# Performance work log

Hardware: AMD Instinct MI355X
Metric: run time of the kernel (lower is better)

The kernel has to match this reference:

```python
import jax, jax.numpy as jnp
import numpy as np

N_HEADS = 16
N_KV_HEADS = 4
N_EMBED = 2048
HEAD_DIM = 128
SECTIONS = [16, 24, 24, 16, 24, 24]


def _process_rotary(c):
    # c: [3, B, T, HEAD_DIM] -> [B, 1, T, HEAD_DIM]
    splits = np.cumsum(SECTIONS)[:-1]
    secs = jnp.split(c, splits, axis=-1)
    out = jnp.concatenate([s[i % 3] for i, s in enumerate(secs)], axis=-1)
    return out[:, None]  # add head axis


def _rotate_half(x):
    x1, x2 = jnp.split(x, 2, axis=-1)
    return jnp.concatenate([-x2, x1], axis=-1)


def setup_inputs() -> dict:
    key = jax.random.key(0)
    ks = jax.random.split(key, 12)
    B, T = 1, 2048
    s = 0.02
    return {
        "x": jax.random.normal(ks[0], (B, T, N_EMBED), jnp.float32),
        "cos": jax.random.uniform(ks[1], (3, B, T, HEAD_DIM), jnp.float32),
        "sin": jax.random.uniform(ks[2], (3, B, T, HEAD_DIM), jnp.float32),
        "Wq": jax.random.normal(ks[3], (N_EMBED, N_EMBED), jnp.float32) * s,
        "bq": jax.random.normal(ks[4], (N_EMBED,), jnp.float32) * s,
        "Wk": jax.random.normal(ks[5], (N_EMBED, N_KV_HEADS * HEAD_DIM), jnp.float32) * s,
        "bk": jax.random.normal(ks[6], (N_KV_HEADS * HEAD_DIM,), jnp.float32) * s,
        "Wv": jax.random.normal(ks[7], (N_EMBED, N_KV_HEADS * HEAD_DIM), jnp.float32) * s,
        "bv": jax.random.normal(ks[8], (N_KV_HEADS * HEAD_DIM,), jnp.float32) * s,
        "Wo": jax.random.normal(ks[9], (N_EMBED, N_EMBED), jnp.float32) * s,
    }


def reference(x, cos, sin, Wq, bq, Wk, bk, Wv, bv, Wo):
    B, T, C = x.shape
    H, Hkv, D = N_HEADS, N_KV_HEADS, HEAD_DIM
    q = (x @ Wq + bq).reshape(B, T, H, D).transpose(0, 2, 1, 3)    # [B,H,T,D]
    k = (x @ Wk + bk).reshape(B, T, Hkv, D).transpose(0, 2, 1, 3)  # [B,Hkv,T,D]
    v = (x @ Wv + bv).reshape(B, T, Hkv, D).transpose(0, 2, 1, 3)
    # multi-section rope (cos/sin are 4-dim -> custom path)
    c = _process_rotary(cos)
    s = _process_rotary(sin)
    q = q * c + _rotate_half(q) * s
    k = k * c + _rotate_half(k) * s
    present_k, present_v = k, v
    # GQA expansion (repeat_interleave over head axis)
    r = H // Hkv
    k = jnp.repeat(k, r, axis=1)
    v = jnp.repeat(v, r, axis=1)
    # causal SDPA
    scores = jnp.einsum("bhqd,bhkd->bhqk", q, k) / jnp.sqrt(jnp.float32(D))
    causal = jnp.tril(jnp.ones((T, T), dtype=bool))
    scores = jnp.where(causal, scores, jnp.finfo(scores.dtype).min)
    attn = jax.nn.softmax(scores, axis=-1)
    y = jnp.einsum("bhqk,bhkd->bhqd", attn, v)
    y = y.transpose(0, 2, 1, 3).reshape(B, T, C)
    y = y @ Wo
    return (y, present_k, present_v)
```

## Files before the change

kernel.cpp:

```cpp
#include <hip/hip_runtime.h>

typedef unsigned short u16;
typedef unsigned int u32;
typedef __attribute__((ext_vector_type(4))) float f32x4;
typedef __attribute__((ext_vector_type(8))) __bf16 bf16x8;
typedef __attribute__((ext_vector_type(4))) u16 u16x4;
typedef __attribute__((ext_vector_type(2))) u32 u32x2;


__device__ __forceinline__ u16 f2bf(float f) {
  union { float f; unsigned u; } v; v.f = f;
  unsigned r = v.u + 0x7fffu + ((v.u >> 16) & 1u);
  return (u16)(r >> 16);
}

__device__ __forceinline__ u32 pack_bf2(float a, float b) {
  union { float f; unsigned u; } x, y;
  x.f = a; y.f = b;
#if __has_builtin(__builtin_amdgcn_perm)
  return __builtin_amdgcn_perm(y.u + 0x8000u, x.u + 0x8000u, 0x07060302u);
#else
  return (u32)((x.u + 0x8000u) >> 16) | ((y.u + 0x8000u) & 0xffff0000u);
#endif
}

__device__ __forceinline__ void stage16(const void* g, void* l) {
#if __has_builtin(__builtin_amdgcn_global_load_lds)
  __builtin_amdgcn_global_load_lds((const __attribute__((address_space(1))) void*)g,
                                   (__attribute__((address_space(3))) void*)l, 16, 0, 0);
#else
  *(f32x4*)l = *(const f32x4*)g;
#endif
}

__device__ __forceinline__ f32x4 mfma16(bf16x8 a, bf16x8 b, f32x4 c) {
  return __builtin_amdgcn_mfma_f32_16x16x32_bf16(a, b, c, 0, 0, 0);
}

__device__ __forceinline__ float fexp2(float x) {
#if __has_builtin(__builtin_amdgcn_exp2f)
  return __builtin_amdgcn_exp2f(x);
#else
  return exp2f(x);
#endif
}

__device__ __forceinline__ int rope_ch(int d) {
  int dd = (d < 64) ? d : d - 64;
  return (dd < 16) ? 0 : (dd < 40 ? 1 : 2);
}


__global__ void yuna_prep(const float* __restrict__ x, u16* __restrict__ xb,
                          const float* __restrict__ cosp, const float* __restrict__ sinp,
                          float* __restrict__ csel, float* __restrict__ ssel,
                          const float* __restrict__ Wq, const float* __restrict__ Wk,
                          const float* __restrict__ Wv, const float* __restrict__ Wo,
                          u16* __restrict__ Wb, u16* __restrict__ Wob) {
  __shared__ float tile[64][65];
  const int bid = blockIdx.x;
  if (bid < 4096) {
    const int mat = bid >> 10;
    const int rem = bid & 1023;
    const float* W;
    u16* out;
    int N;
    if (mat == 0)      { W = Wq; out = Wb;                          N = 2048; }
    else if (mat == 1) { W = Wk; out = Wb + (size_t)2048 * 2048;    N = 512; }
    else if (mat == 2) { W = Wv; out = Wb + (size_t)2560 * 2048;    N = 512; }
    else               { W = Wo; out = Wob;                         N = 2048; }
    int k0 = (rem & 31) << 6, n0 = (rem >> 5) << 6;
    if (n0 >= N) return;
    int tx = threadIdx.x & 63, ty = threadIdx.x >> 6;
#pragma unroll
    for (int j = 0; j < 64; j += 4)
      tile[ty + j][tx] = W[(size_t)(k0 + ty + j) * N + n0 + tx];
    __syncthreads();
#pragma unroll
    for (int j = 0; j < 64; j += 4)
      out[(size_t)(n0 + ty + j) * 2048 + k0 + tx] = f2bf(tile[tx][ty + j]);
  } else if (bid < 8192) {
    int i = (bid - 4096) * 256 + threadIdx.x;
    f32x4 v = ((const f32x4*)x)[i];
    u16x4 o;
    o.x = f2bf(v.x); o.y = f2bf(v.y); o.z = f2bf(v.z); o.w = f2bf(v.w);
    ((u16x4*)xb)[i] = o;
  } else {
    int i = (bid - 8192) * 256 + threadIdx.x;
    int i4 = i * 4;
    int t = i4 >> 7, d = i4 & 127;
    f32x4 c, s;
#pragma unroll
    for (int j = 0; j < 4; ++j) {
      int ch = rope_ch(d + j);
      c[j] = cosp[(size_t)ch * 262144 + (size_t)t * 128 + d + j];
      s[j] = sinp[(size_t)ch * 262144 + (size_t)t * 128 + d + j];
    }
    ((f32x4*)csel)[i] = c;
    ((f32x4*)ssel)[i] = s;
  }
}

__global__ __launch_bounds__(256, 3) void yuna_gemm_qkv(
    const u16* __restrict__ A, const u16* __restrict__ Bt,
    const float* __restrict__ bq, const float* __restrict__ bk, const float* __restrict__ bv,
    const float* __restrict__ csel, const float* __restrict__ ssel,
    u16* __restrict__ qb, u16* __restrict__ kb, u16* __restrict__ vtb,
    float* __restrict__ pk, float* __restrict__ pv) {
  const int K = 2048;
  __shared__ __align__(16) char smem[49152];
  const int tid = threadIdx.x;
  const int wave = tid >> 6, lane = tid & 63;
  const int lrow = lane & 15, lkg = lane >> 4;
  const int m0 = blockIdx.x * 64;
  const int by = blockIdx.y;
  const int n0 = by * 128;
  const int sw = lrow & 7;

  const int srow = tid >> 3;
  const int ssc = (tid & 7) ^ ((tid >> 3) & 7);
  const size_t abase = (size_t)(m0 + srow) * K + ssc * 8;
  const size_t bbase = (size_t)(n0 + srow) * K + ssc * 8;

  const f32x4 fzero = {0.f, 0.f, 0.f, 0.f};
  f32x4 acc[4][2];
#pragma unroll
  for (int mi = 0; mi < 4; ++mi) { acc[mi][0] = fzero; acc[mi][1] = fzero; }

#pragma unroll
  for (int it = 0; it < 2; ++it)
    stage16(A + abase + (size_t)it * 32 * K, smem + (tid + it * 256) * 16);
#pragma unroll
  for (int it = 0; it < 4; ++it)
    stage16(Bt + bbase + (size_t)it * 32 * K, smem + 16384 + (tid + it * 256) * 16);

  for (int k0 = 0, ki = 0; k0 < K; k0 += 64, ++ki) {
    const int cur = ki & 1;
    const char* Asb = smem + cur * 8192;
    const char* Bsb = smem + 16384 + cur * 16384;
    if (k0 + 64 < K) {
      char* Asn = smem + (cur ^ 1) * 8192;
      char* Bsn = smem + 16384 + (cur ^ 1) * 16384;
#pragma unroll
      for (int it = 0; it < 2; ++it)
        stage16(A + abase + (size_t)it * 32 * K + k0 + 64, Asn + (tid + it * 256) * 16);
#pragma unroll
      for (int it = 0; it < 4; ++it)
        stage16(Bt + bbase + (size_t)it * 32 * K + k0 + 64, Bsn + (tid + it * 256) * 16);
      asm volatile("s_waitcnt vmcnt(6)\n\ts_barrier" ::: "memory");
    } else {
      asm volatile("s_waitcnt vmcnt(0)\n\ts_barrier" ::: "memory");
    }
#pragma unroll
    for (int kk = 0; kk < 2; ++kk) {
      const int cof = ((kk * 4 + lkg) ^ sw) << 4;
      bf16x8 af[4], bfr[2];
#pragma unroll
      for (int mi = 0; mi < 4; ++mi)
        af[mi] = *(const bf16x8*)(Asb + (mi * 16 + lrow) * 128 + cof);
#pragma unroll
      for (int ni = 0; ni < 2; ++ni)
        bfr[ni] = *(const bf16x8*)(Bsb + (wave * 16 + ni * 64 + lrow) * 128 + cof);
#pragma unroll
      for (int mi = 0; mi < 4; ++mi)
#pragma unroll
        for (int ni = 0; ni < 2; ++ni)
          acc[mi][ni] = mfma16(af[mi], bfr[ni], acc[mi][ni]);
    }
    asm volatile("s_barrier" ::: "memory");
  }

  if (by >= 20) {
    const int kvh = by - 20;
#pragma unroll
    for (int mi = 0; mi < 4; ++mi)
#pragma unroll
      for (int ni = 0; ni < 2; ++ni) {
        int d = wave * 16 + ni * 64 + lrow;
        float bb = bv[kvh * 128 + d];
        int mb = mi * 16 + lkg * 4;
        float v0 = acc[mi][ni][0] + bb, v1 = acc[mi][ni][1] + bb;
        float v2 = acc[mi][ni][2] + bb, v3 = acc[mi][ni][3] + bb;
        size_t pb = ((size_t)(kvh * 2048 + m0 + mb)) * 128 + d;
        pv[pb] = v0; pv[pb + 128] = v1; pv[pb + 256] = v2; pv[pb + 384] = v3;
        u16x4 w;
        w.x = f2bf(v0); w.y = f2bf(v1); w.z = f2bf(v2); w.w = f2bf(v3);
        *(u16x4*)(vtb + ((size_t)(kvh * 128 + d)) * 2048 + m0 + mb) = w;
      }
  } else {
    const float QSCALE = 1.4426950408889634f * 0.08838834764831845f;
    const bool isQ = (by < 16);
    const int h = isQ ? by : (by - 16);
    const float* bias = isQ ? bq : bk;
    const int dlo = wave * 16 + lrow;
    const float blo = bias[h * 128 + dlo];
    const float bhi = bias[h * 128 + dlo + 64];
#pragma unroll
    for (int mi = 0; mi < 4; ++mi) {
      const int tb = m0 + mi * 16 + lkg * 4;
#pragma unroll
      for (int r = 0; r < 4; ++r) {
        const int t = tb + r;
        float a = acc[mi][0][r] + blo;
        float b = acc[mi][1][r] + bhi;
        size_t cb = (size_t)t * 128 + dlo;
        float cl = csel[cb], sl = ssel[cb];
        float ch = csel[cb + 64], sh = ssel[cb + 64];
        float lo = a * cl - b * sl;
        float hi = b * ch + a * sh;
        size_t o = (((size_t)(h * 2048 + t)) << 7) + dlo;
        if (isQ) {
          qb[o] = f2bf(lo * QSCALE);
          qb[o + 64] = f2bf(hi * QSCALE);
        } else {
          kb[o] = f2bf(lo);
          kb[o + 64] = f2bf(hi);
          pk[o] = lo; pk[o + 64] = hi;
        }
      }
    }
  }
}

__global__ __launch_bounds__(256, 3) void yuna_gemm_out(
    const u16* __restrict__ A, const u16* __restrict__ Bt, float* __restrict__ C) {
  const int K = 2048;
  __shared__ __align__(16) char smem[49152];
  const int tid = threadIdx.x;
  const int wave = tid >> 6, lane = tid & 63;
  const int lrow = lane & 15, lkg = lane >> 4;
  const int m0 = blockIdx.x * 64;
  const int n0 = blockIdx.y * 128;
  const int wc = wave * 32;
  const int sw = lrow & 7;

  const int srow = tid >> 3;
  const int ssc = (tid & 7) ^ ((tid >> 3) & 7);
  const size_t abase = (size_t)(m0 + srow) * K + ssc * 8;
  const size_t bbase = (size_t)(n0 + srow) * K + ssc * 8;

  const f32x4 fzero = {0.f, 0.f, 0.f, 0.f};
  f32x4 acc[4][2];
#pragma unroll
  for (int mi = 0; mi < 4; ++mi) { acc[mi][0] = fzero; acc[mi][1] = fzero; }

#pragma unroll
  for (int it = 0; it < 2; ++it)
    stage16(A + abase + (size_t)it * 32 * K, smem + (tid + it * 256) * 16);
#pragma unroll
  for (int it = 0; it < 4; ++it)
    stage16(Bt + bbase + (size_t)it * 32 * K, smem + 16384 + (tid + it * 256) * 16);

  for (int k0 = 0, ki = 0; k0 < K; k0 += 64, ++ki) {
    const int cur = ki & 1;
    const char* Asb = smem + cur * 8192;
    const char* Bsb = smem + 16384 + cur * 16384;
    if (k0 + 64 < K) {
      char* Asn = smem + (cur ^ 1) * 8192;
      char* Bsn = smem + 16384 + (cur ^ 1) * 16384;
#pragma unroll
      for (int it = 0; it < 2; ++it)
        stage16(A + abase + (size_t)it * 32 * K + k0 + 64, Asn + (tid + it * 256) * 16);
#pragma unroll
      for (int it = 0; it < 4; ++it)
        stage16(Bt + bbase + (size_t)it * 32 * K + k0 + 64, Bsn + (tid + it * 256) * 16);
      asm volatile("s_waitcnt vmcnt(6)\n\ts_barrier" ::: "memory");
    } else {
      asm volatile("s_waitcnt vmcnt(0)\n\ts_barrier" ::: "memory");
    }
#pragma unroll
    for (int kk = 0; kk < 2; ++kk) {
      const int cof = ((kk * 4 + lkg) ^ sw) << 4;
      bf16x8 af[4], bfr[2];
#pragma unroll
      for (int mi = 0; mi < 4; ++mi)
        af[mi] = *(const bf16x8*)(Asb + (mi * 16 + lrow) * 128 + cof);
#pragma unroll
      for (int ni = 0; ni < 2; ++ni)
        bfr[ni] = *(const bf16x8*)(Bsb + (wc + ni * 16 + lrow) * 128 + cof);
#pragma unroll
      for (int mi = 0; mi < 4; ++mi)
#pragma unroll
        for (int ni = 0; ni < 2; ++ni)
          acc[mi][ni] = mfma16(af[mi], bfr[ni], acc[mi][ni]);
    }
    asm volatile("s_barrier" ::: "memory");
  }
#pragma unroll
  for (int mi = 0; mi < 4; ++mi)
#pragma unroll
    for (int ni = 0; ni < 2; ++ni) {
      int d = wc + ni * 16 + lrow;
      int mb = mi * 16 + lkg * 4;
#pragma unroll
      for (int r = 0; r < 4; ++r)
        C[(size_t)(m0 + mb + r) * 2048 + n0 + d] = acc[mi][ni][r];
    }
}

__global__ __launch_bounds__(256, 2) void yuna_flash_attn(
    const u16* __restrict__ Q,
    const u16* __restrict__ Kb,
    const u16* __restrict__ Vt,
    float* __restrict__ OpA,
    float* __restrict__ OpB,
    float* __restrict__ ml) {
  __shared__ __align__(16) u16 Ks[2][64 * 128];
  __shared__ __align__(16) u16 Vs[2][128 * 64];
  __shared__ __align__(16) u16 Ps[64 * 64];
  const int h = blockIdx.x;
  const int yb = blockIdx.y;
  const int qb = 31 - (yb >> 1);
  const int half = yb & 1;
  const int ca = (qb + 2) >> 1;
  const int kb0 = half ? ca : 0;
  const int kb1 = half ? (qb + 1) : ca;
  const int kvh = h >> 2;
  const int tid = threadIdx.x, wave = tid >> 6, lane = tid & 63;
  const int lrow = lane & 15, lkg = lane >> 4;
  const int m = wave * 16 + lrow;
  const int sw = lrow & 7;
  const int qglob = qb * 64 + m;

  const int krow = tid >> 4;
  const int ksc = (tid & 15) ^ ((tid >> 4) & 7);
  const size_t kbase0 = ((size_t)(kvh * 2048 + krow) << 7) + ksc * 8;
  const int vrow = tid >> 3;
  const int vsc = (tid & 7) ^ ((tid >> 3) & 7);
  const size_t vbase0 = (size_t)(kvh * 128 + vrow) * 2048 + vsc * 8;

  bf16x8 qf[4];
#pragma unroll
  for (int kk = 0; kk < 4; ++kk)
    qf[kk] = *(const bf16x8*)(Q + (((size_t)h * 2048 + qglob) << 7) + kk * 32 + lkg * 8);

  const f32x4 fzero = {0.f, 0.f, 0.f, 0.f};
  f32x4 o[8];
#pragma unroll
  for (int dt = 0; dt < 8; ++dt) o[dt] = fzero;
  float m_i = -1e30f, l_i = 0.f;

  if (kb0 < kb1) {
#pragma unroll
    for (int it = 0; it < 4; ++it)
      stage16(Kb + kbase0 + ((size_t)(kb0 * 64 + it * 16) << 7), (char*)Ks[0] + (tid + it * 256) * 16);
#pragma unroll
    for (int it = 0; it < 4; ++it)
      stage16(Vt + vbase0 + (size_t)it * 32 * 2048 + kb0 * 64, (char*)Vs[0] + (tid + it * 256) * 16);

    for (int kb = kb0; kb < kb1; ++kb) {
      const int cur = (kb - kb0) & 1;
      const char* Ksb = (const char*)Ks[cur];
      const char* Vsb = (const char*)Vs[cur];
      if (kb + 1 < kb1) {
        char* Ksn = (char*)Ks[cur ^ 1];
        char* Vsn = (char*)Vs[cur ^ 1];
#pragma unroll
        for (int it = 0; it < 4; ++it)
          stage16(Kb + kbase0 + ((size_t)((kb + 1) * 64 + it * 16) << 7), Ksn + (tid + it * 256) * 16);
#pragma unroll
        for (int it = 0; it < 4; ++it)
          stage16(Vt + vbase0 + (size_t)it * 32 * 2048 + (kb + 1) * 64, Vsn + (tid + it * 256) * 16);
        asm volatile("s_waitcnt vmcnt(8)\n\ts_barrier" ::: "memory");
      } else {
        asm volatile("s_waitcnt vmcnt(0)\n\ts_barrier" ::: "memory");
      }

      f32x4 s[4];
#pragma unroll
      for (int nt = 0; nt < 4; ++nt) s[nt] = fzero;
      __builtin_amdgcn_s_setprio(1);
#pragma unroll
      for (int kk = 0; kk < 4; ++kk) {
        const int cof = ((kk * 4 + lkg) ^ sw) << 4;
        bf16x8 kf[4];
#pragma unroll
        for (int nt = 0; nt < 4; ++nt)
          kf[nt] = *(const bf16x8*)(Ksb + (nt * 16 + lrow) * 256 + cof);
#pragma unroll
        for (int nt = 0; nt < 4; ++nt)
          s[nt] = mfma16(kf[nt], qf[kk], s[nt]);
      }
      __builtin_amdgcn_s_setprio(0);
      if (kb == qb) {
        const int kbase = kb * 64 + lkg * 4;
#pragma unroll
        for (int nt = 0; nt < 4; ++nt)
#pragma unroll
          for (int r = 0; r < 4; ++r)
            if (kbase + nt * 16 + r > qglob) s[nt][r] = -1e30f;
      }

      float mxl = -1e30f;
#pragma unroll
      for (int nt = 0; nt < 4; ++nt)
#pragma unroll
        for (int r = 0; r < 4; ++r) mxl = fmaxf(mxl, s[nt][r]);
      if (__any(mxl > m_i + 8.0f)) {
        float mx = fmaxf(mxl, __shfl_xor(mxl, 16));
        mx = fmaxf(mx, __shfl_xor(mx, 32));
        float mnew = fmaxf(m_i, mx);
        float alpha = fexp2(m_i - mnew);
        m_i = mnew;
        l_i *= alpha;
#pragma unroll
        for (int dt = 0; dt < 8; ++dt) o[dt] *= alpha;
      }
      float ps = 0.f;
      const int hh = lkg & 1;
#pragma unroll
      for (int nt = 0; nt < 4; ++nt) {
        float p0 = fexp2(s[nt][0] - m_i);
        float p1 = fexp2(s[nt][1] - m_i);
        float p2 = fexp2(s[nt][2] - m_i);
        float p3 = fexp2(s[nt][3] - m_i);
        ps += (p0 + p1) + (p2 + p3);
        u32x2 pk2;
        pk2.x = pack_bf2(p0, p1);
        pk2.y = pack_bf2(p2, p3);
        int cc = 2 * nt + (lkg >> 1);
        *(u32x2*)((char*)Ps + m * 128 + ((cc ^ (m & 7)) << 4) + hh * 8) = pk2;
      }
      l_i += ps;

      __builtin_amdgcn_s_setprio(1);
#pragma unroll
      for (int kk = 0; kk < 2; ++kk) {
        const int cof = ((kk * 4 + lkg) ^ sw) << 4;
        bf16x8 pf = *(const bf16x8*)((char*)Ps + m * 128 + cof);
        bf16x8 vf[8];
#pragma unroll
        for (int dt = 0; dt < 8; ++dt)
          vf[dt] = *(const bf16x8*)(Vsb + (dt * 16 + lrow) * 128 + cof);
#pragma unroll
        for (int dt = 0; dt < 8; ++dt)
          o[dt] = mfma16(vf[dt], pf, o[dt]);
      }
      __builtin_amdgcn_s_setprio(0);
      asm volatile("s_barrier" ::: "memory");
    }
  }

  l_i += __shfl_xor(l_i, 16);
  l_i += __shfl_xor(l_i, 32);
  size_t row = (size_t)h * 2048 + qglob;
  if (lkg == 0)
    *(float2*)(ml + ((size_t)(half << 15) + row) * 2) = float2{m_i, l_i};
  float* orow = (half ? OpB : OpA) + row * 128 + lkg * 4;
#pragma unroll
  for (int dt = 0; dt < 8; ++dt)
    *(f32x4*)(orow + dt * 16) = o[dt];
}

__global__ void yuna_merge(const float* __restrict__ OpA, const float* __restrict__ OpB,
                           const float* __restrict__ ml, u16* __restrict__ Y) {
  int idx = blockIdx.x * 256 + threadIdx.x;
  int d4 = idx & 31;
  int t = (idx >> 5) & 2047;
  int h = idx >> 16;
  size_t row = (size_t)h * 2048 + t;
  float2 a2 = *(const float2*)(ml + row * 2);
  float2 b2 = *(const float2*)(ml + (32768 + row) * 2);
  float M = fmaxf(a2.x, b2.x);
  float wA = fexp2(a2.x - M), wB = fexp2(b2.x - M);
  float inv = 1.f / (a2.y * wA + b2.y * wB);
  wA *= inv; wB *= inv;
  f32x4 a = ((const f32x4*)OpA)[row * 32 + d4];
  f32x4 b = ((const f32x4*)OpB)[row * 32 + d4];
  u16x4 w;
  w.x = f2bf(a[0] * wA + b[0] * wB);
  w.y = f2bf(a[1] * wA + b[1] * wB);
  w.z = f2bf(a[2] * wA + b[2] * wB);
  w.w = f2bf(a[3] * wA + b[3] * wB);
  *(u16x4*)(Y + (size_t)t * 2048 + h * 128 + d4 * 4) = w;
}


extern "C" void kernel_launch(void* const* d_in, const int* in_sizes, int n_in,
                              void* d_out, int out_size, void* d_ws, size_t ws_size,
                              hipStream_t stream) {
  const float* x = (const float*)d_in[0];
  const float* cosp = (const float*)d_in[1];
  const float* sinp = (const float*)d_in[2];
  const float* Wq = (const float*)d_in[3];
  const float* bq = (const float*)d_in[4];
  const float* Wk = (const float*)d_in[5];
  const float* bk = (const float*)d_in[6];
  const float* Wv = (const float*)d_in[7];
  const float* bv = (const float*)d_in[8];
  const float* Wo = (const float*)d_in[9];
  float* out = (float*)d_out;
  float* out_k = out + 4194304;
  float* out_v = out + 5242880;

  char* ws = (char*)d_ws;
  u16* xb   = (u16*)(ws + 0);
  u16* Wb   = (u16*)(ws + 8388608);
  u16* Wob  = (u16*)(ws + 20971520);
  float* csel = (float*)(ws + 29360128);
  float* ssel = (float*)(ws + 30408704);
  u16* qbuf = (u16*)(ws + 54525952);
  u16* kbuf = (u16*)(ws + 62914560);
  u16* vtb  = (u16*)(ws + 65011712);
  u16* yat  = (u16*)(ws + 67108864);
  float* opA = (float*)(ws + 0);
  float* mlb = (float*)(ws + 17825792);
  float* opB = (float*)(ws + 31457280);

  yuna_prep<<<8448, 256, 0, stream>>>(x, xb, cosp, sinp, csel, ssel,
                                      Wq, Wk, Wv, Wo, Wb, Wob);
  yuna_gemm_qkv<<<dim3(32, 24), 256, 0, stream>>>(xb, Wb, bq, bk, bv, csel, ssel,
                                                  qbuf, kbuf, vtb, out_k, out_v);
  yuna_flash_attn<<<dim3(16, 64), 256, 0, stream>>>(qbuf, kbuf, vtb, opA, opB, mlb);
  yuna_merge<<<4096, 256, 0, stream>>>(opA, opB, mlb, yat);
  yuna_gemm_out<<<dim3(32, 16), 256, 0, stream>>>(yat, Wob, out);
}
```

Measured before the change: 217.4 us.

## Fuse split-KV merge into flash attention via last-arriver atomic counter

Removes the separate merge kernel. Each attention block writes its partial output and (m, l) stats, then bumps a per-(head, query-block) counter with an atomic. Whichever of the two split halves arrives second reads the other's partial, combines them, and writes the bf16 output directly. This saves a kernel launch and one pass over the partial buffers, but adds a thread fence, two block barriers and a flag reset in the prep kernel.

```diff
diff --git a/kernel.cpp b/kernel.cpp
--- a/kernel.cpp
+++ b/kernel.cpp
@@ -56,7 +56,8 @@
                           float* __restrict__ csel, float* __restrict__ ssel,
                           const float* __restrict__ Wq, const float* __restrict__ Wk,
                           const float* __restrict__ Wv, const float* __restrict__ Wo,
-                          u16* __restrict__ Wb, u16* __restrict__ Wob) {
+                          u16* __restrict__ Wb, u16* __restrict__ Wob,
+                          int* __restrict__ flags) {
   __shared__ float tile[64][65];
   const int bid = blockIdx.x;
   if (bid < 4096) {
@@ -85,7 +86,7 @@
     u16x4 o;
     o.x = f2bf(v.x); o.y = f2bf(v.y); o.z = f2bf(v.z); o.w = f2bf(v.w);
     ((u16x4*)xb)[i] = o;
-  } else {
+  } else if (bid < 8448) {
     int i = (bid - 8192) * 256 + threadIdx.x;
     int i4 = i * 4;
     int t = i4 >> 7, d = i4 & 127;
@@ -98,6 +99,9 @@
     }
     ((f32x4*)csel)[i] = c;
     ((f32x4*)ssel)[i] = s;
+  } else {
+    flags[threadIdx.x] = 0;
+    flags[threadIdx.x + 256] = 0;
   }
 }
 
@@ -304,10 +308,13 @@
     const u16* __restrict__ Vt,
     float* __restrict__ OpA,
     float* __restrict__ OpB,
-    float* __restrict__ ml) {
+    float* __restrict__ ml,
+    int* __restrict__ flags,
+    u16* __restrict__ Y) {
   __shared__ __align__(16) u16 Ks[2][64 * 128];
   __shared__ __align__(16) u16 Vs[2][128 * 64];
   __shared__ __align__(16) u16 Ps[64 * 64];
+  __shared__ int who;
   const int h = blockIdx.x;
   const int yb = blockIdx.y;
   const int qb = 31 - (yb >> 1);
@@ -443,36 +450,38 @@
 
   l_i += __shfl_xor(l_i, 16);
   l_i += __shfl_xor(l_i, 32);
-  size_t row = (size_t)h * 2048 + qglob;
+  const size_t row = (size_t)h * 2048 + qglob;
   if (lkg == 0)
     *(float2*)(ml + ((size_t)(half << 15) + row) * 2) = float2{m_i, l_i};
-  float* orow = (half ? OpB : OpA) + row * 128 + lkg * 4;
-#pragma unroll
-  for (int dt = 0; dt < 8; ++dt)
-    *(f32x4*)(orow + dt * 16) = o[dt];
-}
-
-__global__ void yuna_merge(const float* __restrict__ OpA, const float* __restrict__ OpB,
-                           const float* __restrict__ ml, u16* __restrict__ Y) {
-  int idx = blockIdx.x * 256 + threadIdx.x;
-  int d4 = idx & 31;
-  int t = (idx >> 5) & 2047;
-  int h = idx >> 16;
-  size_t row = (size_t)h * 2048 + t;
-  float2 a2 = *(const float2*)(ml + row * 2);
-  float2 b2 = *(const float2*)(ml + (32768 + row) * 2);
-  float M = fmaxf(a2.x, b2.x);
-  float wA = fexp2(a2.x - M), wB = fexp2(b2.x - M);
-  float inv = 1.f / (a2.y * wA + b2.y * wB);
-  wA *= inv; wB *= inv;
-  f32x4 a = ((const f32x4*)OpA)[row * 32 + d4];
-  f32x4 b = ((const f32x4*)OpB)[row * 32 + d4];
-  u16x4 w;
-  w.x = f2bf(a[0] * wA + b[0] * wB);
-  w.y = f2bf(a[1] * wA + b[1] * wB);
-  w.z = f2bf(a[2] * wA + b[2] * wB);
-  w.w = f2bf(a[3] * wA + b[3] * wB);
-  *(u16x4*)(Y + (size_t)t * 2048 + h * 128 + d4 * 4) = w;
+  {
+    float* orow = (half ? OpB : OpA) + row * 128 + lkg * 4;
+#pragma unroll
+    for (int dt = 0; dt < 8; ++dt)
+      *(f32x4*)(orow + dt * 16) = o[dt];
+  }
+  __threadfence();
+  __syncthreads();
+  if (tid == 0) who = atomicAdd(&flags[h * 32 + qb], 1);
+  __syncthreads();
+  if (who == 1) {
+    __threadfence();
+    float2 p2 = *(const float2*)(ml + ((size_t)((1 - half) << 15) + row) * 2);
+    float M = fmaxf(m_i, p2.x);
+    float wO = fexp2(m_i - M), wP = fexp2(p2.x - M);
+    float inv = 1.f / (l_i * wO + p2.y * wP);
+    wO *= inv; wP *= inv;
+    const float* prow = (half ? OpA : OpB) + row * 128 + lkg * 4;
+#pragma unroll
+    for (int dt = 0; dt < 8; ++dt) {
+      f32x4 p = *(const f32x4*)(prow + dt * 16);
+      u16x4 w;
+      w.x = f2bf(o[dt][0] * wO + p[0] * wP);
+      w.y = f2bf(o[dt][1] * wO + p[1] * wP);
+      w.z = f2bf(o[dt][2] * wO + p[2] * wP);
+      w.w = f2bf(o[dt][3] * wO + p[3] * wP);
+      *(u16x4*)(Y + (size_t)qglob * 2048 + h * 128 + dt * 16 + lkg * 4) = w;
+    }
+  }
 }
 
 
@@ -506,12 +515,13 @@
   float* opA = (float*)(ws + 0);
   float* mlb = (float*)(ws + 17825792);
   float* opB = (float*)(ws + 31457280);
-
-  yuna_prep<<<8448, 256, 0, stream>>>(x, xb, cosp, sinp, csel, ssel,
-                                      Wq, Wk, Wv, Wo, Wb, Wob);
+  int* flags = (int*)(ws + 75497472);
+
+  yuna_prep<<<8449, 256, 0, stream>>>(x, xb, cosp, sinp, csel, ssel,
+                                      Wq, Wk, Wv, Wo, Wb, Wob, flags);
   yuna_gemm_qkv<<<dim3(32, 24), 256, 0, stream>>>(xb, Wb, bq, bk, bv, csel, ssel,
                                                   qbuf, kbuf, vtb, out_k, out_v);
-  yuna_flash_attn<<<dim3(16, 64), 256, 0, stream>>>(qbuf, kbuf, vtb, opA, opB, mlb);
-  yuna_merge<<<4096, 256, 0, stream>>>(opA, opB, mlb, yat);
+  yuna_flash_attn<<<dim3(16, 64), 256, 0, stream>>>(qbuf, kbuf, vtb, opA, opB, mlb,
+                                                    flags, yat);
   yuna_gemm_out<<<dim3(32, 16), 256, 0, stream>>>(yat, Wob, out);
 }
```

Measured after the change: 412.2 us. 1.9x slower.

## Use 128-row query tiles with 512 threads and three-way KV split

Applied to the files above, without the earlier changes.

Flash attention blocks now process 128 query rows with 8 waves, so each staged K/V tile is shared across twice as many queries. The KV range is split three ways per query block instead of two, and the merge kernel combines three partial outputs. This is meant to halve K/V reloads per query and balance causal work, at the cost of a third partial buffer, extra merge traffic and higher per-block resource use.

```diff
diff --git a/kernel.cpp b/kernel.cpp
--- a/kernel.cpp
+++ b/kernel.cpp
@@ -298,35 +298,36 @@
     }
 }
 
-__global__ __launch_bounds__(256, 2) void yuna_flash_attn(
+__global__ __launch_bounds__(512, 4) void yuna_flash_attn(
     const u16* __restrict__ Q,
     const u16* __restrict__ Kb,
     const u16* __restrict__ Vt,
-    float* __restrict__ OpA,
-    float* __restrict__ OpB,
+    float* __restrict__ Op0,
+    float* __restrict__ Op1,
+    float* __restrict__ Op2,
     float* __restrict__ ml) {
   __shared__ __align__(16) u16 Ks[2][64 * 128];
   __shared__ __align__(16) u16 Vs[2][128 * 64];
-  __shared__ __align__(16) u16 Ps[64 * 64];
+  __shared__ __align__(16) u16 Ps[128 * 64];
   const int h = blockIdx.x;
   const int yb = blockIdx.y;
-  const int qb = 31 - (yb >> 1);
-  const int half = yb & 1;
-  const int ca = (qb + 2) >> 1;
-  const int kb0 = half ? ca : 0;
-  const int kb1 = half ? (qb + 1) : ca;
+  const int qq = 15 - yb / 3;
+  const int c = yb % 3;
+  const int T = 2 * qq + 2;
+  const int kb0 = c * T / 3;
+  const int kb1 = (c + 1) * T / 3;
   const int kvh = h >> 2;
   const int tid = threadIdx.x, wave = tid >> 6, lane = tid & 63;
   const int lrow = lane & 15, lkg = lane >> 4;
   const int m = wave * 16 + lrow;
   const int sw = lrow & 7;
-  const int qglob = qb * 64 + m;
+  const int qglob = qq * 128 + m;
 
   const int krow = tid >> 4;
-  const int ksc = (tid & 15) ^ ((tid >> 4) & 7);
+  const int ksc = (tid & 15) ^ (krow & 7);
   const size_t kbase0 = ((size_t)(kvh * 2048 + krow) << 7) + ksc * 8;
   const int vrow = tid >> 3;
-  const int vsc = (tid & 7) ^ ((tid >> 3) & 7);
+  const int vsc = (tid & 7) ^ (vrow & 7);
   const size_t vbase0 = (size_t)(kvh * 128 + vrow) * 2048 + vsc * 8;
 
   bf16x8 qf[4];
@@ -342,11 +343,11 @@
 
   if (kb0 < kb1) {
 #pragma unroll
-    for (int it = 0; it < 4; ++it)
-      stage16(Kb + kbase0 + ((size_t)(kb0 * 64 + it * 16) << 7), (char*)Ks[0] + (tid + it * 256) * 16);
-#pragma unroll
-    for (int it = 0; it < 4; ++it)
-      stage16(Vt + vbase0 + (size_t)it * 32 * 2048 + kb0 * 64, (char*)Vs[0] + (tid + it * 256) * 16);
+    for (int it = 0; it < 2; ++it)
+      stage16(Kb + kbase0 + ((size_t)(kb0 * 64 + it * 32) << 7), (char*)Ks[0] + (tid + it * 512) * 16);
+#pragma unroll
+    for (int it = 0; it < 2; ++it)
+      stage16(Vt + vbase0 + (size_t)it * 64 * 2048 + kb0 * 64, (char*)Vs[0] + (tid + it * 512) * 16);
 
     for (int kb = kb0; kb < kb1; ++kb) {
       const int cur = (kb - kb0) & 1;
@@ -356,12 +357,12 @@
         char* Ksn = (char*)Ks[cur ^ 1];
         char* Vsn = (char*)Vs[cur ^ 1];
 #pragma unroll
-        for (int it = 0; it < 4; ++it)
-          stage16(Kb + kbase0 + ((size_t)((kb + 1) * 64 + it * 16) << 7), Ksn + (tid + it * 256) * 16);
-#pragma unroll
-        for (int it = 0; it < 4; ++it)
-          stage16(Vt + vbase0 + (size_t)it * 32 * 2048 + (kb + 1) * 64, Vsn + (tid + it * 256) * 16);
-        asm volatile("s_waitcnt vmcnt(8)\n\ts_barrier" ::: "memory");
+        for (int it = 0; it < 2; ++it)
+          stage16(Kb + kbase0 + ((size_t)((kb + 1) * 64 + it * 32) << 7), Ksn + (tid + it * 512) * 16);
+#pragma unroll
+        for (int it = 0; it < 2; ++it)
+          stage16(Vt + vbase0 + (size_t)it * 64 * 2048 + (kb + 1) * 64, Vsn + (tid + it * 512) * 16);
+        asm volatile("s_waitcnt vmcnt(4)\n\ts_barrier" ::: "memory");
       } else {
         asm volatile("s_waitcnt vmcnt(0)\n\ts_barrier" ::: "memory");
       }
@@ -382,13 +383,13 @@
           s[nt] = mfma16(kf[nt], qf[kk], s[nt]);
       }
       __builtin_amdgcn_s_setprio(0);
-      if (kb == qb) {
+      if (kb >= 2 * qq) {
         const int kbase = kb * 64 + lkg * 4;
 #pragma unroll
         for (int nt = 0; nt < 4; ++nt)
 #pragma unroll
           for (int r = 0; r < 4; ++r)
-            if (kbase + nt * 16 + r > qglob) s[nt][r] = -1e30f;
+            if (kbase + nt * 16 + r > qglob) s[nt][r] = -3e38f;
       }
 
       float mxl = -1e30f;
@@ -443,17 +444,19 @@
 
   l_i += __shfl_xor(l_i, 16);
   l_i += __shfl_xor(l_i, 32);
-  size_t row = (size_t)h * 2048 + qglob;
+  const size_t row = (size_t)h * 2048 + qglob;
   if (lkg == 0)
-    *(float2*)(ml + ((size_t)(half << 15) + row) * 2) = float2{m_i, l_i};
-  float* orow = (half ? OpB : OpA) + row * 128 + lkg * 4;
+    *(float2*)(ml + ((size_t)(c * 32768) + row) * 2) = float2{m_i, l_i};
+  float* Op = (c == 0) ? Op0 : (c == 1 ? Op1 : Op2);
+  float* orow = Op + row * 128 + lkg * 4;
 #pragma unroll
   for (int dt = 0; dt < 8; ++dt)
     *(f32x4*)(orow + dt * 16) = o[dt];
 }
 
-__global__ void yuna_merge(const float* __restrict__ OpA, const float* __restrict__ OpB,
-                           const float* __restrict__ ml, u16* __restrict__ Y) {
+__global__ void yuna_merge(const float* __restrict__ Op0, const float* __restrict__ Op1,
+                           const float* __restrict__ Op2, const float* __restrict__ ml,
+                           u16* __restrict__ Y) {
   int idx = blockIdx.x * 256 + threadIdx.x;
   int d4 = idx & 31;
   int t = (idx >> 5) & 2047;
@@ -461,17 +464,19 @@
   size_t row = (size_t)h * 2048 + t;
   float2 a2 = *(const float2*)(ml + row * 2);
   float2 b2 = *(const float2*)(ml + (32768 + row) * 2);
-  float M = fmaxf(a2.x, b2.x);
-  float wA = fexp2(a2.x - M), wB = fexp2(b2.x - M);
-  float inv = 1.f / (a2.y * wA + b2.y * wB);
-  wA *= inv; wB *= inv;
-  f32x4 a = ((const f32x4*)OpA)[row * 32 + d4];
-  f32x4 b = ((const f32x4*)OpB)[row * 32 + d4];
+  float2 c2 = *(const float2*)(ml + (65536 + row) * 2);
+  float M = fmaxf(fmaxf(a2.x, b2.x), c2.x);
+  float wA = fexp2(a2.x - M), wB = fexp2(b2.x - M), wC = fexp2(c2.x - M);
+  float inv = 1.f / (a2.y * wA + b2.y * wB + c2.y * wC);
+  wA *= inv; wB *= inv; wC *= inv;
+  f32x4 a = ((const f32x4*)Op0)[row * 32 + d4];
+  f32x4 b = ((const f32x4*)Op1)[row * 32 + d4];
+  f32x4 cc = ((const f32x4*)Op2)[row * 32 + d4];
   u16x4 w;
-  w.x = f2bf(a[0] * wA + b[0] * wB);
-  w.y = f2bf(a[1] * wA + b[1] * wB);
-  w.z = f2bf(a[2] * wA + b[2] * wB);
-  w.w = f2bf(a[3] * wA + b[3] * wB);
+  w.x = f2bf(a[0] * wA + b[0] * wB + cc[0] * wC);
+  w.y = f2bf(a[1] * wA + b[1] * wB + cc[1] * wC);
+  w.z = f2bf(a[2] * wA + b[2] * wB + cc[2] * wC);
+  w.w = f2bf(a[3] * wA + b[3] * wB + cc[3] * wC);
   *(u16x4*)(Y + (size_t)t * 2048 + h * 128 + d4 * 4) = w;
 }
 
@@ -503,15 +508,16 @@
   u16* kbuf = (u16*)(ws + 62914560);
   u16* vtb  = (u16*)(ws + 65011712);
   u16* yat  = (u16*)(ws + 67108864);
-  float* opA = (float*)(ws + 0);
+  float* op0 = (float*)(ws + 0);
   float* mlb = (float*)(ws + 17825792);
-  float* opB = (float*)(ws + 31457280);
+  float* op1 = (float*)(ws + 31457280);
+  float* op2 = (float*)(ws + 79691776);
 
   yuna_prep<<<8448, 256, 0, stream>>>(x, xb, cosp, sinp, csel, ssel,
                                       Wq, Wk, Wv, Wo, Wb, Wob);
   yuna_gemm_qkv<<<dim3(32, 24), 256, 0, stream>>>(xb, Wb, bq, bk, bv, csel, ssel,
                                                   qbuf, kbuf, vtb, out_k, out_v);
-  yuna_flash_attn<<<dim3(16, 64), 256, 0, stream>>>(qbuf, kbuf, vtb, opA, opB, mlb);
-  yuna_merge<<<4096, 256, 0, stream>>>(opA, opB, mlb, yat);
+  yuna_flash_attn<<<dim3(16, 48), 512, 0, stream>>>(qbuf, kbuf, vtb, op0, op1, op2, mlb);
+  yuna_merge<<<4096, 256, 0, stream>>>(op0, op1, op2, mlb, yat);
   yuna_gemm_out<<<dim3(32, 16), 256, 0, stream>>>(yat, Wob, out);
 }
```

Result: no change. 220.3 us (+1.3%).
